# Kernel optimization log

Hardware: AMD Instinct MI355X
Metric: run time of the kernel (lower is better)

## Reference

```python
import jax, jax.numpy as jnp
import numpy as np

N, M, F0, FB, F, H, NC, NCONV = 60000, 12, 92, 41, 64, 128, 2000, 3
EPS = 1e-5


def setup_inputs() -> dict:
    key = jax.random.key(0)
    ks = jax.random.split(key, 12)
    s = 0.05
    return {
        "atom_fea": jax.random.normal(ks[0], (N, F0), jnp.float32),
        "nbr_fea": jax.random.normal(ks[1], (N, M, FB), jnp.float32),
        "nbr_fea_idx": jax.random.randint(ks[2], (N, M), 0, N),
        "crystal_atom_idx": jnp.sort(jax.random.randint(ks[3], (N,), 0, NC)),
        "W_emb": jax.random.normal(ks[4], (F0, F), jnp.float32) * s,
        "b_emb": jnp.zeros((F,), jnp.float32),
        "W_full": jax.random.normal(ks[5], (NCONV, 2 * F + FB, 2 * F), jnp.float32) * s,
        "b_full": jnp.zeros((NCONV, 2 * F), jnp.float32),
        "g1": jnp.ones((NCONV, 2 * F), jnp.float32),
        "be1": jnp.zeros((NCONV, 2 * F), jnp.float32),
        "g2": jnp.ones((NCONV, F), jnp.float32),
        "be2": jnp.zeros((NCONV, F), jnp.float32),
        "W_fc": jax.random.normal(ks[6], (F, H), jnp.float32) * s,
        "b_fc": jnp.zeros((H,), jnp.float32),
        "W_out": jax.random.normal(ks[7], (H, 1), jnp.float32) * s,
        "b_out": jnp.zeros((1,), jnp.float32),
    }


def _bn(x, g, b):
    # training-mode batch norm over leading (row) dim
    m = x.mean(axis=0)
    v = x.var(axis=0)
    return (x - m) * jax.lax.rsqrt(v + EPS) * g + b


def _conv_layer(x, nbr_fea, nbr_fea_idx, Wf, bf, g1, be1, g2, be2):
    n, m = nbr_fea_idx.shape
    f = x.shape[1]
    atom_nbr = x[nbr_fea_idx]  # (N, M, F) gather
    total = jnp.concatenate(
        [jnp.broadcast_to(x[:, None, :], (n, m, f)), atom_nbr, nbr_fea], axis=2
    )  # (N, M, 2F+FB)
    gated = total @ Wf + bf  # (N, M, 2F)
    gated = _bn(gated.reshape(-1, 2 * f), g1, be1).reshape(n, m, 2 * f)
    nbr_filter, nbr_core = jnp.split(gated, 2, axis=2)
    summed = jnp.sum(jax.nn.sigmoid(nbr_filter) * jax.nn.softplus(nbr_core), axis=1)
    summed = _bn(summed, g2, be2)
    return jax.nn.softplus(x + summed)


def reference(atom_fea, nbr_fea, nbr_fea_idx, crystal_atom_idx, W_emb, b_emb,
              W_full, b_full, g1, be1, g2, be2, W_fc, b_fc, W_out, b_out):
    x = atom_fea @ W_emb + b_emb  # (N, F)
    for i in range(NCONV):
        x = _conv_layer(x, nbr_fea, nbr_fea_idx, W_full[i], b_full[i],
                        g1[i], be1[i], g2[i], be2[i])
    # mean-pool atoms per crystal (segment mean)
    sums = jax.ops.segment_sum(x, crystal_atom_idx, num_segments=NC)
    cnt = jax.ops.segment_sum(jnp.ones((x.shape[0],), x.dtype), crystal_atom_idx,
                              num_segments=NC)
    crys = sums / jnp.maximum(cnt, 1.0)[:, None]  # (NC, F)
    crys = jax.nn.softplus(crys) @ W_fc + b_fc
    crys = jax.nn.softplus(crys)
    return crys @ W_out + b_out  # (NC, 1)
```

## Files before the change

kernel.cpp:

```cpp
#include <hip/hip_runtime.h>
#include <hip/hip_bf16.h>


#define NATOM 60000
#define MNBR  12
#define F0D   92
#define FBD   41
#define FD    64
#define F2D   128
#define NCRY  2000
#define HD    128
#define NSUP  15000

#define OFF_X      0ull
#define OFF_XH     3840000ull
#define OFF_SUMMED 5760000ull
#define OFF_STATS  9600000ull
#define OFF_CRYS   9600384ull
#define OFF_CNT    9728384ull
#define OFF_WCONV  9730384ull
#define OFF_WBF    9811220ull
#define OFF_FLAG   9848084ull
#define WS_NEED_BYTES (9848085ull * 4ull)

#define W_EMB_O  0
#define B_EMB_O  5888
#define W_FULL_O 5952
#define B_FULL_O 70848
#define G1_O     71232
#define BE1_O    71616
#define G2_O     72000
#define BE2_O    72192
#define W_FC_O   72384
#define B_FC_O   80576
#define W_OUT_O  80704
#define B_OUT_O  80832
#define WC_TOTAL 80833

typedef unsigned short u16;
typedef __attribute__((ext_vector_type(8))) short bf16x8;
typedef __attribute__((ext_vector_type(4))) float f32x4;

__device__ __forceinline__ float bf2f(u16 u){
  union { unsigned int i; float f; } v; v.i = ((unsigned int)u) << 16; return v.f;
}
__device__ __forceinline__ u16 f2bf(float f){
  union { float f; unsigned int i; } v; v.f = f;
  unsigned int x = v.i;
  return (u16)((x + 0x7FFFu + ((x >> 16) & 1u)) >> 16);
}
__device__ __forceinline__ float softplusf_(float x){
  return fmaxf(x, 0.f) + log1pf(expf(-fabsf(x)));
}
__device__ __forceinline__ float softplus_fast(float x){
  return fmaxf(x, 0.f) + __logf(1.f + __expf(-fabsf(x)));
}
__device__ __forceinline__ float sigmoid_fast(float x){
  return __builtin_amdgcn_rcpf(1.f + __expf(-x));
}

__global__ __launch_bounds__(64) void detect_kernel(
    const u16* __restrict__ data, int* __restrict__ flag){
  int tid = threadIdx.x;
  float v = bf2f(data[tid * 2]);
  float av = fabsf(v);
  bool sane = (av > 1e-6f) && (av < 100.f);
  unsigned long long m = __ballot(sane);
  if (tid == 0) *flag = (__popcll(m) >= 32) ? 1 : 0;
}

struct CvtArgs {
  const void* src[12];
  int start[13];
};

__global__ __launch_bounds__(256) void cvt_all_kernel(
    CvtArgs a, float* __restrict__ dst, const int* __restrict__ flag){
  int i = blockIdx.x * 256 + threadIdx.x;
  if (i >= WC_TOTAL) return;
  int r = 0;
  while (i >= a.start[r + 1]) r++;
  int rel = i - a.start[r];
  if (*flag) dst[i] = bf2f(((const u16*)a.src[r])[rel]);
  else       dst[i] = ((const float*)a.src[r])[rel];
}

__global__ __launch_bounds__(256) void build_bfrag(
    const float* __restrict__ wfull, u16* __restrict__ wbf){
  int t = blockIdx.x * 256 + threadIdx.x;
  if (t >= 3 * 6 * 8 * 64) return;
  int lane = t & 63, nt = (t >> 6) & 7, c = (t >> 9) % 6, layer = t / 3072;
  int q = lane >> 4, nloc = lane & 15;
  u16 vals[8];
  #pragma unroll
  for (int i = 0; i < 8; i++){
    int k = c * 32 + q * 8 + i;
    float v = (k < 169) ? wfull[layer * 169 * F2D + k * F2D + nt * 16 + nloc] : 0.f;
    vals[i] = f2bf(v);
  }
  *(uint4*)&wbf[(size_t)t * 8] = *(uint4*)vals;
}

__global__ __launch_bounds__(256) void embed_kernel(
    const void* __restrict__ atom_fea, const float* __restrict__ W_emb,
    const float* __restrict__ b_emb, float* __restrict__ x,
    u16* __restrict__ xh, const int* __restrict__ flag){
  int tid = threadIdx.x;
  int n = blockIdx.x * 4 + (tid >> 6);
  int f = tid & 63;
  float acc = b_emb[f];
  if (*flag){
    const u16* arow = (const u16*)atom_fea + n * F0D;
    for (int k = 0; k < F0D; k++)
      acc = fmaf(bf2f(arow[k]), W_emb[k * FD + f], acc);
  } else {
    const float* arow = (const float*)atom_fea + n * F0D;
    for (int k = 0; k < F0D; k++)
      acc = fmaf(arow[k], W_emb[k * FD + f], acc);
  }
  x[n * FD + f] = acc;
  xh[n * FD + f] = f2bf(acc);
}

template<int ACT>
__global__ __launch_bounds__(256, 3) void conv_mfma(
    const u16* __restrict__ xh, const void* __restrict__ nbr_fea,
    const int* __restrict__ nbr_idx, const u16* __restrict__ wbf_l,
    const float* __restrict__ bfull, const float* __restrict__ sum1,
    const float* __restrict__ sq1, const float* __restrict__ g1,
    const float* __restrict__ be1, float* __restrict__ summed,
    float* __restrict__ o_sum, float* __restrict__ o_sq,
    const int* __restrict__ flag){
  extern __shared__ char smem[];
  u16*   bond = (u16*)smem;
  float* gbuf = (float*)(smem + 4096);
  float* redS = ACT ? (gbuf + 48 * 128) : gbuf;
  float* redQ = redS + (ACT ? 64 : 128);

  const int tid = threadIdx.x;
  const int w = tid >> 6, lane = tid & 63;
  const int q = lane >> 4, nloc = lane & 15, q8 = q * 8;
  const int isbf = *flag;

  bf16x8 Bf[6][2];
  const bf16x8* Bv = (const bf16x8*)wbf_l;
  #pragma unroll
  for (int c = 0; c < 6; c++)
    #pragma unroll
    for (int t2 = 0; t2 < 2; t2++)
      Bf[c][t2] = Bv[(c * 8 + w * 2 + t2) * 64 + lane];
  float bias0 = bfull[w * 32 + nloc];
  float bias1 = bfull[w * 32 + 16 + nloc];

  float A0 = 0.f, B0 = 0.f, A1 = 0.f, B1 = 0.f;
  if (ACT){
    const float invR = 1.f / (float)(NATOM * MNBR);
    float m0 = sum1[lane] * invR;
    float v0 = fmaxf(sq1[lane] * invR - m0 * m0, 0.f);
    A0 = g1[lane] * rsqrtf(v0 + 1e-5f);  B0 = be1[lane] - m0 * A0;
    float m1 = sum1[64 + lane] * invR;
    float v1 = fmaxf(sq1[64 + lane] * invR - m1 * m1, 0.f);
    A1 = g1[64 + lane] * rsqrtf(v1 + 1e-5f);  B1 = be1[64 + lane] - m1 * A1;
  }
  float sAcc0 = 0.f, sAcc1 = 0.f, qAcc0 = 0.f, qAcc1 = 0.f;
  if (tid < (ACT ? 64 : 128)){ redS[tid] = 0.f; redQ[tid] = 0.f; }

  const bf16x8* xv = (const bf16x8*)xh;
  for (int s = blockIdx.x; s < NSUP; s += gridDim.x){
    if (isbf){
      const uint4* src = (const uint4*)((const u16*)nbr_fea + (size_t)s * 1968);
      if (tid < 246) *(uint4*)&bond[tid * 8] = src[tid];
    } else {
      const float4* src = (const float4*)((const float*)nbr_fea + (size_t)s * 1968);
      for (int t = tid; t < 492; t += 256){
        float4 v = src[t];
        ushort4 o; o.x = f2bf(v.x); o.y = f2bf(v.y); o.z = f2bf(v.z); o.w = f2bf(v.w);
        *(ushort4*)&bond[t * 4] = o;
      }
    }
    __syncthreads();
    #pragma unroll
    for (int et = 0; et < 3; et++){
      int e  = s * 48 + et * 16 + nloc;
      int na = s * 4 + (et * 16 + nloc) / 12;
      int nb = nbr_idx[e];
      bf16x8 a0 = xv[na * 8 + q];
      bf16x8 a1 = xv[na * 8 + 4 + q];
      bf16x8 a2 = xv[nb * 8 + q];
      bf16x8 a3 = xv[nb * 8 + 4 + q];
      int ebase = (et * 16 + nloc) * 41;
      bf16x8 a4, a5;
      #pragma unroll
      for (int i = 0; i < 8; i++){
        a4[i] = (short)bond[ebase + q8 + i];
        int k5 = 32 + q8 + i;
        u16 v5 = bond[ebase + ((k5 < 41) ? k5 : 0)];
        a5[i] = (k5 < 41) ? (short)v5 : (short)0;
      }
      #pragma unroll
      for (int t2 = 0; t2 < 2; t2++){
        float bs = t2 ? bias1 : bias0;
        f32x4 acc = {bs, bs, bs, bs};
        acc = __builtin_amdgcn_mfma_f32_16x16x32_bf16(a0, Bf[0][t2], acc, 0, 0, 0);
        acc = __builtin_amdgcn_mfma_f32_16x16x32_bf16(a1, Bf[1][t2], acc, 0, 0, 0);
        acc = __builtin_amdgcn_mfma_f32_16x16x32_bf16(a2, Bf[2][t2], acc, 0, 0, 0);
        acc = __builtin_amdgcn_mfma_f32_16x16x32_bf16(a3, Bf[3][t2], acc, 0, 0, 0);
        acc = __builtin_amdgcn_mfma_f32_16x16x32_bf16(a4, Bf[4][t2], acc, 0, 0, 0);
        acc = __builtin_amdgcn_mfma_f32_16x16x32_bf16(a5, Bf[5][t2], acc, 0, 0, 0);
        if (ACT){
          int col = w * 32 + t2 * 16 + nloc;
          int r0 = et * 16 + q * 4;
          gbuf[(r0 + 0) * 128 + col] = acc[0];
          gbuf[(r0 + 1) * 128 + col] = acc[1];
          gbuf[(r0 + 2) * 128 + col] = acc[2];
          gbuf[(r0 + 3) * 128 + col] = acc[3];
        } else {
          float ss = acc[0] + acc[1] + acc[2] + acc[3];
          float qq = acc[0]*acc[0] + acc[1]*acc[1] + acc[2]*acc[2] + acc[3]*acc[3];
          if (t2){ sAcc1 += ss; qAcc1 += qq; } else { sAcc0 += ss; qAcc0 += qq; }
        }
      }
    }
    if (ACT){
      __syncthreads();
      float p = 0.f;
      #pragma unroll
      for (int m = 0; m < 12; m++){
        int el = w * 12 + m;
        float u = fmaf(gbuf[el * 128 + lane],      A0, B0);
        float v = fmaf(gbuf[el * 128 + 64 + lane], A1, B1);
        p = fmaf(sigmoid_fast(u), softplus_fast(v), p);
      }
      summed[(s * 4 + w) * 64 + lane] = p;
      sAcc0 += p;  qAcc0 = fmaf(p, p, qAcc0);
    }
    __syncthreads();
  }
  if (ACT){
    atomicAdd(&redS[lane], sAcc0);
    atomicAdd(&redQ[lane], qAcc0);
    __syncthreads();
    if (tid < 64){ atomicAdd(&o_sum[tid], redS[tid]); atomicAdd(&o_sq[tid], redQ[tid]); }
  } else {
    int c0 = w * 32 + nloc;
    atomicAdd(&redS[c0], sAcc0);       atomicAdd(&redQ[c0], qAcc0);
    atomicAdd(&redS[c0 + 16], sAcc1);  atomicAdd(&redQ[c0 + 16], qAcc1);
    __syncthreads();
    if (tid < 128){ atomicAdd(&o_sum[tid], redS[tid]); atomicAdd(&o_sq[tid], redQ[tid]); }
  }
}

__global__ __launch_bounds__(256) void update_x_kernel(
    float* __restrict__ x, u16* __restrict__ xh,
    const float* __restrict__ summed,
    const float* __restrict__ sum2, const float* __restrict__ sq2,
    const float* __restrict__ g2, const float* __restrict__ be2){
  int idx = blockIdx.x * 256 + threadIdx.x;
  int f = idx & 63;
  const float invN = 1.f / (float)NATOM;
  float mean = sum2[f] * invN;
  float var  = fmaxf(sq2[f] * invN - mean * mean, 0.f);
  float a = g2[f] * rsqrtf(var + 1e-5f);
  float b = be2[f] - mean * a;
  float v = x[idx] + fmaf(summed[idx], a, b);
  float r = softplusf_(v);
  x[idx] = r;
  xh[idx] = f2bf(r);
}

__global__ __launch_bounds__(256) void pool_kernel(
    const float* __restrict__ x, const int* __restrict__ cidx,
    float* __restrict__ crys, float* __restrict__ cnt){
  int idx = blockIdx.x * 256 + threadIdx.x;
  int n = idx >> 6, f = idx & 63;
  int c = cidx[n];
  atomicAdd(&crys[c * FD + f], x[idx]);
  if (f == 0) atomicAdd(&cnt[c], 1.f);
}

__global__ __launch_bounds__(128) void head_kernel(
    const float* __restrict__ crys, const float* __restrict__ cnt,
    const float* __restrict__ W_fc, const float* __restrict__ b_fc,
    const float* __restrict__ W_out, const float* __restrict__ b_out,
    void* __restrict__ out, const int* __restrict__ flag){
  __shared__ float p_s[FD];
  __shared__ float red_s[HD];
  int c = blockIdx.x, tid = threadIdx.x;
  if (tid < FD){
    float ct = fmaxf(cnt[c], 1.f);
    p_s[tid] = softplusf_(crys[c * FD + tid] / ct);
  }
  __syncthreads();
  float acc = b_fc[tid];
  for (int k = 0; k < FD; k++)
    acc = fmaf(p_s[k], W_fc[k * HD + tid], acc);
  float h = softplusf_(acc);
  red_s[tid] = h * W_out[tid];
  __syncthreads();
  for (int s = HD / 2; s > 0; s >>= 1){
    if (tid < s) red_s[tid] += red_s[tid + s];
    __syncthreads();
  }
  if (tid == 0){
    float r = red_s[0] + b_out[0];
    if (*flag) ((u16*)out)[c] = f2bf(r);
    else       ((float*)out)[c] = r;
  }
}

extern "C" void kernel_launch(void* const* d_in, const int* in_sizes, int n_in,
                              void* d_out, int out_size, void* d_ws, size_t ws_size,
                              hipStream_t stream){
  if (ws_size < WS_NEED_BYTES) return;
  const void* atom_fea = d_in[0];
  const void* nbr_fea  = d_in[1];
  const int* nbr_idx   = (const int*)d_in[2];
  const int* cidx      = (const int*)d_in[3];

  float* ws     = (float*)d_ws;
  float* x      = ws + OFF_X;
  u16*   xh     = (u16*)(ws + OFF_XH);
  float* summed = ws + OFF_SUMMED;
  float* sum1   = ws + OFF_STATS;
  float* sq1    = sum1 + 128;
  float* sum2   = sq1 + 128;
  float* sq2    = sum2 + 64;
  float* crys   = ws + OFF_CRYS;
  float* cnt    = ws + OFF_CNT;
  float* wc     = ws + OFF_WCONV;
  u16*   wbf    = (u16*)(ws + OFF_WBF);
  int*   flag   = (int*)(ws + OFF_FLAG);

  detect_kernel<<<1, 64, 0, stream>>>((const u16*)nbr_fea, flag);
  CvtArgs ca;
  const int srcidx[12] = {4,5,6,7,8,9,10,11,12,13,14,15};
  const int starts[13] = {W_EMB_O, B_EMB_O, W_FULL_O, B_FULL_O, G1_O, BE1_O,
                          G2_O, BE2_O, W_FC_O, B_FC_O, W_OUT_O, B_OUT_O, WC_TOTAL};
  for (int i = 0; i < 12; i++){ ca.src[i] = d_in[srcidx[i]]; ca.start[i] = starts[i]; }
  ca.start[12] = WC_TOTAL;
  cvt_all_kernel<<<(WC_TOTAL + 255) / 256, 256, 0, stream>>>(ca, wc, flag);
  build_bfrag<<<(9216 + 255) / 256, 256, 0, stream>>>(wc + W_FULL_O, wbf);

  embed_kernel<<<NATOM / 4, 256, 0, stream>>>(atom_fea, wc + W_EMB_O, wc + B_EMB_O,
                                              x, xh, flag);
  for (int i = 0; i < 3; i++){
    const u16* wbf_l = wbf + (size_t)i * 3072 * 8;
    hipMemsetAsync(sum1, 0, 384 * sizeof(float), stream);
    conv_mfma<0><<<1024, 256, 5120, stream>>>(xh, nbr_fea, nbr_idx, wbf_l,
        wc + B_FULL_O + i * F2D, sum1, sq1, wc + G1_O + i * F2D,
        wc + BE1_O + i * F2D, summed, sum1, sq1, flag);
    conv_mfma<1><<<1024, 256, 29184, stream>>>(xh, nbr_fea, nbr_idx, wbf_l,
        wc + B_FULL_O + i * F2D, sum1, sq1, wc + G1_O + i * F2D,
        wc + BE1_O + i * F2D, summed, sum2, sq2, flag);
    update_x_kernel<<<(NATOM * FD) / 256, 256, 0, stream>>>(x, xh, summed, sum2, sq2,
        wc + G2_O + i * FD, wc + BE2_O + i * FD);
  }
  hipMemsetAsync(crys, 0, (NCRY * FD + NCRY) * sizeof(float), stream);
  pool_kernel<<<(NATOM * FD) / 256, 256, 0, stream>>>(x, cidx, crys, cnt);
  head_kernel<<<NCRY, 128, 0, stream>>>(crys, cnt, wc + W_FC_O, wc + B_FC_O,
      wc + W_OUT_O, wc + B_OUT_O, d_out, flag);
}
```

Baseline: 1.173 ms.

## Pre-pack bond MFMA fragments in LDS, pad gbuf, hoist neighbor index loads, enlarge grid

After: 1.100 ms. 1.07x faster.

```diff
diff --git a/kernel.cpp b/kernel.cpp
--- a/kernel.cpp
+++ b/kernel.cpp
@@ -11,6 +11,7 @@
 #define NCRY  2000
 #define HD    128
 #define NSUP  15000
+#define GS    132
 
 #define OFF_X      0ull
 #define OFF_XH     3840000ull
@@ -132,10 +133,10 @@
     float* __restrict__ o_sum, float* __restrict__ o_sq,
     const int* __restrict__ flag){
   extern __shared__ char smem[];
-  u16*   bond = (u16*)smem;
-  float* gbuf = (float*)(smem + 4096);
-  float* redS = ACT ? (gbuf + 48 * 128) : gbuf;
-  float* redQ = redS + (ACT ? 64 : 128);
+  u16*   fragA = (u16*)smem;
+  float* gbuf  = (float*)(smem + 6144);
+  float* redS  = ACT ? (gbuf + 48 * GS) : (float*)(smem + 6144);
+  float* redQ  = redS + (ACT ? 64 : 128);
 
   const int tid = threadIdx.x;
   const int w = tid >> 6, lane = tid & 63;
@@ -167,36 +168,44 @@
 
   const bf16x8* xv = (const bf16x8*)xh;
   for (int s = blockIdx.x; s < NSUP; s += gridDim.x){
-    if (isbf){
-      const uint4* src = (const uint4*)((const u16*)nbr_fea + (size_t)s * 1968);
-      if (tid < 246) *(uint4*)&bond[tid * 8] = src[tid];
-    } else {
-      const float4* src = (const float4*)((const float*)nbr_fea + (size_t)s * 1968);
-      for (int t = tid; t < 492; t += 256){
-        float4 v = src[t];
-        ushort4 o; o.x = f2bf(v.x); o.y = f2bf(v.y); o.z = f2bf(v.z); o.w = f2bf(v.w);
-        *(ushort4*)&bond[t * 4] = o;
+    if (w < 3){
+      size_t eg = (size_t)(s * 48 + w * 16 + nloc);
+      u16 v4[8], v5[8];
+      if (isbf){
+        const u16* br = (const u16*)nbr_fea + eg * 41;
+        #pragma unroll
+        for (int i = 0; i < 8; i++) v4[i] = br[q8 + i];
+        #pragma unroll
+        for (int i = 0; i < 8; i++){
+          int k5 = 32 + q8 + i;
+          v5[i] = (k5 < 41) ? br[(k5 < 41) ? k5 : 0] : (u16)0;
+        }
+      } else {
+        const float* br = (const float*)nbr_fea + eg * 41;
+        #pragma unroll
+        for (int i = 0; i < 8; i++) v4[i] = f2bf(br[q8 + i]);
+        #pragma unroll
+        for (int i = 0; i < 8; i++){
+          int k5 = 32 + q8 + i;
+          v5[i] = (k5 < 41) ? f2bf(br[(k5 < 41) ? k5 : 0]) : (u16)0;
+        }
       }
+      *(uint4*)&fragA[(w * 2 + 0) * 512 + lane * 8] = *(uint4*)v4;
+      *(uint4*)&fragA[(w * 2 + 1) * 512 + lane * 8] = *(uint4*)v5;
     }
+    int e0 = s * 48 + nloc;
+    int nb0 = nbr_idx[e0], nb1 = nbr_idx[e0 + 16], nb2 = nbr_idx[e0 + 32];
     __syncthreads();
     #pragma unroll
     for (int et = 0; et < 3; et++){
-      int e  = s * 48 + et * 16 + nloc;
+      int nb = (et == 0) ? nb0 : (et == 1) ? nb1 : nb2;
       int na = s * 4 + (et * 16 + nloc) / 12;
-      int nb = nbr_idx[e];
       bf16x8 a0 = xv[na * 8 + q];
       bf16x8 a1 = xv[na * 8 + 4 + q];
       bf16x8 a2 = xv[nb * 8 + q];
       bf16x8 a3 = xv[nb * 8 + 4 + q];
-      int ebase = (et * 16 + nloc) * 41;
-      bf16x8 a4, a5;
-      #pragma unroll
-      for (int i = 0; i < 8; i++){
-        a4[i] = (short)bond[ebase + q8 + i];
-        int k5 = 32 + q8 + i;
-        u16 v5 = bond[ebase + ((k5 < 41) ? k5 : 0)];
-        a5[i] = (k5 < 41) ? (short)v5 : (short)0;
-      }
+      bf16x8 a4 = *(bf16x8*)&fragA[(et * 2 + 0) * 512 + lane * 8];
+      bf16x8 a5 = *(bf16x8*)&fragA[(et * 2 + 1) * 512 + lane * 8];
       #pragma unroll
       for (int t2 = 0; t2 < 2; t2++){
         float bs = t2 ? bias1 : bias0;
@@ -210,10 +219,10 @@
         if (ACT){
           int col = w * 32 + t2 * 16 + nloc;
           int r0 = et * 16 + q * 4;
-          gbuf[(r0 + 0) * 128 + col] = acc[0];
-          gbuf[(r0 + 1) * 128 + col] = acc[1];
-          gbuf[(r0 + 2) * 128 + col] = acc[2];
-          gbuf[(r0 + 3) * 128 + col] = acc[3];
+          gbuf[(r0 + 0) * GS + col] = acc[0];
+          gbuf[(r0 + 1) * GS + col] = acc[1];
+          gbuf[(r0 + 2) * GS + col] = acc[2];
+          gbuf[(r0 + 3) * GS + col] = acc[3];
         } else {
           float ss = acc[0] + acc[1] + acc[2] + acc[3];
           float qq = acc[0]*acc[0] + acc[1]*acc[1] + acc[2]*acc[2] + acc[3]*acc[3];
@@ -227,8 +236,8 @@
       #pragma unroll
       for (int m = 0; m < 12; m++){
         int el = w * 12 + m;
-        float u = fmaf(gbuf[el * 128 + lane],      A0, B0);
-        float v = fmaf(gbuf[el * 128 + 64 + lane], A1, B1);
+        float u = fmaf(gbuf[el * GS + lane],      A0, B0);
+        float v = fmaf(gbuf[el * GS + 64 + lane], A1, B1);
         p = fmaf(sigmoid_fast(u), softplus_fast(v), p);
       }
       summed[(s * 4 + w) * 64 + lane] = p;
@@ -343,13 +352,15 @@
 
   embed_kernel<<<NATOM / 4, 256, 0, stream>>>(atom_fea, wc + W_EMB_O, wc + B_EMB_O,
                                               x, xh, flag);
+  const int LDS_STATS = 6144 + 2 * 128 * 4;
+  const int LDS_ACT   = 6144 + (48 * GS + 128) * 4;
   for (int i = 0; i < 3; i++){
     const u16* wbf_l = wbf + (size_t)i * 3072 * 8;
     hipMemsetAsync(sum1, 0, 384 * sizeof(float), stream);
-    conv_mfma<0><<<1024, 256, 5120, stream>>>(xh, nbr_fea, nbr_idx, wbf_l,
+    conv_mfma<0><<<3000, 256, LDS_STATS, stream>>>(xh, nbr_fea, nbr_idx, wbf_l,
         wc + B_FULL_O + i * F2D, sum1, sq1, wc + G1_O + i * F2D,
         wc + BE1_O + i * F2D, summed, sum1, sq1, flag);
-    conv_mfma<1><<<1024, 256, 29184, stream>>>(xh, nbr_fea, nbr_idx, wbf_l,
+    conv_mfma<1><<<3000, 256, LDS_ACT, stream>>>(xh, nbr_fea, nbr_idx, wbf_l,
         wc + B_FULL_O + i * F2D, sum1, sq1, wc + G1_O + i * F2D,
         wc + BE1_O + i * F2D, summed, sum2, sq2, flag);
     update_x_kernel<<<(NATOM * FD) / 256, 256, 0, stream>>>(x, xh, summed, sum2, sq2,
```
